# Kernel tuning notes

Measured on AMD Instinct MI355X. Metric: run time of the kernel, lower is better.

## Reference

```python
import jax, jax.numpy as jnp
import numpy as np

N_NODES = 50000
N_EDGES = 1_600_000
F_IN = 128
HID = 64
HEADS = 4
NCLS = 2
NEG_SLOPE = 0.2  # PyG GATConv default


def setup_inputs() -> dict:
    key = jax.random.key(0)
    ks = jax.random.split(key, 12)
    s = 0.1
    return {
        "x": jax.random.normal(ks[0], (N_NODES, F_IN), jnp.float32),
        "edge_index": jax.random.randint(ks[1], (2, N_EDGES), 0, N_NODES, jnp.int32),
        "W1": jax.random.normal(ks[2], (F_IN, HEADS * HID), jnp.float32) * s,
        "att_src1": jax.random.normal(ks[3], (HEADS, HID), jnp.float32) * s,
        "att_dst1": jax.random.normal(ks[4], (HEADS, HID), jnp.float32) * s,
        "b1": jnp.zeros((HEADS * HID,), jnp.float32),
        "W2": jax.random.normal(ks[5], (HEADS * HID, HID), jnp.float32) * s,
        "att_src2": jax.random.normal(ks[6], (1, HID), jnp.float32) * s,
        "att_dst2": jax.random.normal(ks[7], (1, HID), jnp.float32) * s,
        "b2": jnp.zeros((HID,), jnp.float32),
        "Wc": jax.random.normal(ks[8], (HID, NCLS), jnp.float32) * s,
        "bc": jnp.zeros((NCLS,), jnp.float32),
    }


def _gat_layer(x, src, dst, W, a_src, a_dst, bias, heads, out_ch, concat):
    """Faithful PyG GATConv (eval mode): gather, LeakyReLU score, segment softmax by dst, scatter-add."""
    n = x.shape[0]
    h = (x @ W).reshape(n, heads, out_ch)            # [N, H, C]
    alpha_s = (h * a_src).sum(-1)                    # [N, H]
    alpha_d = (h * a_dst).sum(-1)                    # [N, H]
    e = jax.nn.leaky_relu(alpha_s[src] + alpha_d[dst], NEG_SLOPE)  # [E, H]
    e_max = jax.ops.segment_max(e, dst, num_segments=n)
    ex = jnp.exp(e - e_max[dst])
    denom = jax.ops.segment_sum(ex, dst, num_segments=n)
    coef = ex / (denom[dst] + 1e-16)                 # [E, H]
    out = jax.ops.segment_sum(h[src] * coef[:, :, None], dst, num_segments=n)  # [N, H, C]
    out = out.reshape(n, heads * out_ch) if concat else out.mean(axis=1)
    return out + bias


def reference(x, edge_index, W1, att_src1, att_dst1, b1, W2, att_src2, att_dst2, b2, Wc, bc):
    n = x.shape[0]
    loop = jnp.arange(n, dtype=edge_index.dtype)     # GATConv add_self_loops=True
    src = jnp.concatenate([edge_index[0], loop])
    dst = jnp.concatenate([edge_index[1], loop])
    h1 = jax.nn.elu(_gat_layer(x, src, dst, W1, att_src1, att_dst1, b1, HEADS, HID, True))
    # dropout p=0.6 is identity in eval mode
    h2 = jax.nn.elu(_gat_layer(h1, src, dst, W2, att_src2, att_dst2, b2, 1, HID, False))
    pooled = h2.mean(axis=0, keepdims=True)          # batch=None path: [1, HID]
    return pooled @ Wc + bc                          # [1, NCLS]
```

## Files before the change

### kernel.cpp

```cpp
#include <hip/hip_runtime.h>
#include <cstdint>
#include <cstddef>

#define NEG_SLOPE 0.2f
#define F_IN 128
#define C1 256
#define HID 64
#define HEADS 4
#define LOG2E 1.4426950408889634f
#define NBUCK 196
#define BCAP 10240

typedef __attribute__((ext_vector_type(8))) short bf16x8;
typedef __attribute__((ext_vector_type(4))) float f32x4;
typedef __attribute__((ext_vector_type(2))) float f32x2;
typedef unsigned long long ull;

__device__ __forceinline__ float wave_reduce_sum(float v) {
#pragma unroll
  for (int off = 32; off > 0; off >>= 1) v += __shfl_down(v, off);
  return v;
}

__device__ __forceinline__ unsigned short f2bf(float f) {
  union { float f; unsigned int u; } v; v.f = f;
  unsigned int u = v.u;
  unsigned int r = (u + 0x7fffu + ((u >> 16) & 1u)) >> 16;
  return (unsigned short)r;
}

__device__ __forceinline__ unsigned char f2fp8(float f) {
  int p = __builtin_amdgcn_cvt_pk_fp8_f32(f, f, 0, false);
  return (unsigned char)(p & 0xff);
}

__global__ __launch_bounds__(256) void setup_kernel(const float* __restrict__ W1,
                                                    const float* __restrict__ W2,
                                                    unsigned short* __restrict__ W1b,
                                                    unsigned short* __restrict__ W2b,
                                                    int* __restrict__ gcursor,
                                                    float* __restrict__ poolrep) {
  const int TOT = 256 + 4096 + 32768 + 16384;
  for (int idx = threadIdx.x + blockIdx.x * 256; idx < TOT; idx += 256 * gridDim.x) {
    if (idx < 256) {
      gcursor[idx] = 0;
    } else if (idx < 256 + 4096) {
      poolrep[idx - 256] = 0.f;
    } else if (idx < 256 + 4096 + 32768) {
      int o = idx - (256 + 4096);
      int head = o >> 13, ks = (o >> 11) & 3, nt = (o >> 9) & 3;
      int lane = (o >> 3) & 63, j = o & 7;
      int k = ks * 32 + (lane >> 4) * 8 + j;
      int c = head * 64 + nt * 16 + (lane & 15);
      W1b[o] = f2bf(W1[k * 256 + c]);
    } else {
      int o = idx - (256 + 4096 + 32768);
      int ks = o >> 11, nt = (o >> 9) & 3, lane = (o >> 3) & 63, j = o & 7;
      int k = ks * 32 + (lane >> 4) * 8 + j;
      int c = nt * 16 + (lane & 15);
      W2b[o] = f2bf(W2[k * 64 + c]);
    }
  }
}

__global__ __launch_bounds__(256) void gemm1_partition(const float* __restrict__ Af,
                                                       const unsigned short* __restrict__ Wb,
                                                       unsigned char* __restrict__ H8,
                                                       float* __restrict__ as_out,
                                                       float* __restrict__ ad_out,
                                                       const float* __restrict__ att_s,
                                                       const float* __restrict__ att_d,
                                                       int M, int rowblocks,
                                                       const int* __restrict__ esrc,
                                                       const int* __restrict__ edst,
                                                       int* __restrict__ gcursor,
                                                       unsigned* __restrict__ pairs,
                                                       int E, int Etot) {
  __shared__ int hist[256];
  __shared__ int base[256];
  if (blockIdx.x < rowblocks) {
    constexpr int KSTEPS = 4, NH = HEADS, K = 128, N = 256;
    const int lane = threadIdx.x & 63, wid = threadIdx.x >> 6;
    const int rowbase = blockIdx.x * 64 + wid * 16;
    const int g = lane >> 4, li = lane & 15;
    int r_a = rowbase + li;
    if (r_a > M - 1) r_a = M - 1;

    f32x4 acc[NH][4];
#pragma unroll
    for (int h = 0; h < NH; h++)
#pragma unroll
      for (int nt = 0; nt < 4; nt++) {
        acc[h][nt][0] = 0.f; acc[h][nt][1] = 0.f; acc[h][nt][2] = 0.f; acc[h][nt][3] = 0.f;
      }

#pragma unroll
    for (int ks = 0; ks < KSTEPS; ks++) {
      bf16x8 a;
      const float* p = Af + (size_t)r_a * K + ks * 32 + g * 8;
      float4 v0 = *(const float4*)p, v1 = *(const float4*)(p + 4);
      a[0] = (short)f2bf(v0.x); a[1] = (short)f2bf(v0.y);
      a[2] = (short)f2bf(v0.z); a[3] = (short)f2bf(v0.w);
      a[4] = (short)f2bf(v1.x); a[5] = (short)f2bf(v1.y);
      a[6] = (short)f2bf(v1.z); a[7] = (short)f2bf(v1.w);
#pragma unroll
      for (int h = 0; h < NH; h++)
#pragma unroll
        for (int nt = 0; nt < 4; nt++) {
          bf16x8 b = *(const bf16x8*)(Wb + ((size_t)((h * KSTEPS + ks) * 4 + nt) * 64 + lane) * 8);
          acc[h][nt] = __builtin_amdgcn_mfma_f32_16x16x32_bf16(a, b, acc[h][nt], 0, 0, 0);
        }
    }

#pragma unroll
    for (int h = 0; h < NH; h++) {
      float asum[4] = {0.f, 0.f, 0.f, 0.f}, dsum[4] = {0.f, 0.f, 0.f, 0.f};
#pragma unroll
      for (int nt = 0; nt < 4; nt++) {
        float ws = att_s[h * 64 + nt * 16 + li];
        float wd = att_d[h * 64 + nt * 16 + li];
#pragma unroll
        for (int r = 0; r < 4; r++) { asum[r] += acc[h][nt][r] * ws; dsum[r] += acc[h][nt][r] * wd; }
      }
#pragma unroll
      for (int r = 0; r < 4; r++) {
#pragma unroll
        for (int m = 1; m < 16; m <<= 1) {
          asum[r] += __shfl_xor(asum[r], m);
          dsum[r] += __shfl_xor(dsum[r], m);
        }
      }
#pragma unroll
      for (int r = 0; r < 4; r++) {
        int gr = rowbase + g * 4 + r;
        if (gr < M) {
#pragma unroll
          for (int nt = 0; nt < 4; nt++)
            H8[(size_t)gr * N + h * 64 + nt * 16 + li] = f2fp8(acc[h][nt][r]);
          if (li == 0) {
            as_out[(size_t)gr * NH + h] = asum[r] * LOG2E;
            ad_out[(size_t)gr * NH + h] = dsum[r] * LOG2E;
          }
        }
      }
    }
  } else {
    const int tid = threadIdx.x;
    const int e0 = (blockIdx.x - rowblocks) * 2048;
    hist[tid] = 0;
    __syncthreads();
    int d8[8], rk8[8], bk8[8];
#pragma unroll
    for (int j = 0; j < 8; j++) {
      int e = e0 + tid * 8 + j;
      d8[j] = -1;
      if (e < Etot) {
        int d = (e < E) ? edst[e] : (e - E);
        d8[j] = d;
        bk8[j] = d >> 8;
        rk8[j] = atomicAdd(&hist[bk8[j]], 1);
      }
    }
    __syncthreads();
    if (hist[tid] > 0) base[tid] = atomicAdd(&gcursor[tid], hist[tid]);
    __syncthreads();
#pragma unroll
    for (int j = 0; j < 8; j++) {
      int e = e0 + tid * 8 + j;
      if (e < Etot) {
        int s = (e < E) ? esrc[e] : (e - E);
        pairs[(size_t)bk8[j] * BCAP + base[bk8[j]] + rk8[j]] =
            (unsigned)s | ((unsigned)(d8[j] & 255) << 16);
      }
    }
  }
}

__global__ __launch_bounds__(512) void bucket_csr(const unsigned* __restrict__ pairs,
                                                  const int* __restrict__ gcursor,
                                                  const float4* __restrict__ as1,
                                                  const float4* __restrict__ ad1,
                                                  unsigned short* __restrict__ src16,
                                                  ull* __restrict__ w4,
                                                  int* __restrict__ row_ptr,
                                                  int N, int Etot) {
  __shared__ int hist[256], offs[256], cnt2[256], gpre[256];
  const int b = blockIdx.x;
  const int tid = threadIdx.x;
  if (tid < 256) {
    hist[tid] = 0; cnt2[tid] = 0;
    gpre[tid] = (tid < NBUCK) ? gcursor[tid] : 0;
  }
  __syncthreads();
  for (int off = 1; off < 256; off <<= 1) {
    int t = 0;
    if (tid < 256 && tid >= off) t = gpre[tid - off];
    __syncthreads();
    if (tid < 256) gpre[tid] += t;
    __syncthreads();
  }
  const int cnt = gcursor[b];
  const int gbase = (b == 0) ? 0 : gpre[b - 1];
  const unsigned* bp = pairs + (size_t)b * BCAP;
  if (b == 0 && tid == 0) row_ptr[N] = Etot;

  for (int i = tid; i < cnt; i += 512) {
    unsigned p = bp[i];
    atomicAdd(&hist[p >> 16], 1);
  }
  __syncthreads();
  if (tid < 256) offs[tid] = hist[tid];
  __syncthreads();
  for (int off = 1; off < 256; off <<= 1) {
    int t = 0;
    if (tid < 256 && tid >= off) t = offs[tid - off];
    __syncthreads();
    if (tid < 256) offs[tid] += t;
    __syncthreads();
  }
  if (tid < 256) {
    int node = b * 256 + tid;
    if (node < N) row_ptr[node] = gbase + offs[tid] - hist[tid];
  }
  __syncthreads();
  for (int i = tid; i < cnt; i += 512) {
    unsigned p = bp[i];
    int lo = (int)(p >> 16);
    int src = (int)(p & 0xffffu);
    int rank = atomicAdd(&cnt2[lo], 1);
    int pos = gbase + offs[lo] - hist[lo] + rank;
    float4 a = as1[src], dd = ad1[b * 256 + lo];
    float s0 = a.x + dd.x, s1 = a.y + dd.y, s2 = a.z + dd.z, s3 = a.w + dd.w;
    float w0 = exp2f(fmaxf(s0, NEG_SLOPE * s0));
    float w1 = exp2f(fmaxf(s1, NEG_SLOPE * s1));
    float w2 = exp2f(fmaxf(s2, NEG_SLOPE * s2));
    float w3 = exp2f(fmaxf(s3, NEG_SLOPE * s3));
    unsigned w01 = (unsigned)f2bf(w0) | ((unsigned)f2bf(w1) << 16);
    unsigned w23 = (unsigned)f2bf(w2) | ((unsigned)f2bf(w3) << 16);
    src16[pos] = (unsigned short)src;
    w4[pos] = (ull)w01 | ((ull)w23 << 32);
  }
}

__global__ __launch_bounds__(256) void agg1_gemm2(const unsigned char* __restrict__ H8,
                                                  const unsigned short* __restrict__ src16,
                                                  const ull* __restrict__ w4,
                                                  const int* __restrict__ row_ptr,
                                                  const float* __restrict__ b1,
                                                  const unsigned short* __restrict__ W2b,
                                                  const float* __restrict__ att_s2,
                                                  const float* __restrict__ att_d2,
                                                  unsigned char* __restrict__ H2,
                                                  float* __restrict__ as2,
                                                  float* __restrict__ ad2, int n) {
  __shared__ unsigned char lds_h[16 * 512];
  __shared__ float pA[4][16], pD[4][16];
  const int tid = threadIdx.x;
  const int l = tid & 63, w = tid >> 6;
  const int dbase = blockIdx.x * 16;
  const int hh = l >> 4;
  const int shamt = (hh & 1) ? 0 : 16;
  const bool lowpair = hh < 2;
  const float4 bb = *(const float4*)(b1 + l * 4);

#define WSEL(wv) __uint_as_float((((lowpair) ? (unsigned)(wv) : (unsigned)((wv) >> 32)) << shamt) & 0xffff0000u)
#define ACCUM(wgt, u8)                                                     \
  {                                                                        \
    f32x2 lo_ = __builtin_amdgcn_cvt_pk_f32_fp8((int)(u8), false);         \
    f32x2 hi_ = __builtin_amdgcn_cvt_pk_f32_fp8((int)(u8), true);          \
    accA += lo_ * (wgt); accB += hi_ * (wgt);                              \
    denom += (wgt);                                                        \
  }
  for (int i = 0; i < 4; i++) {
    int dloc = w * 4 + i;
    int d = dbase + dloc;
    bool active = d < n;
    f32x2 accA = {0.f, 0.f}, accB = {0.f, 0.f};
    float denom = 0.f;
    if (active) {
      int e0 = __builtin_amdgcn_readfirstlane(row_ptr[d]);
      int e1 = __builtin_amdgcn_readfirstlane(row_ptr[d + 1]);
      int e = e0;
      for (; e + 7 < e1; e += 8) {
        unsigned s0 = src16[e],     s1 = src16[e + 1];
        unsigned s2 = src16[e + 2], s3 = src16[e + 3];
        unsigned s4 = src16[e + 4], s5 = src16[e + 5];
        unsigned s6 = src16[e + 6], s7 = src16[e + 7];
        ull wv0 = w4[e],     wv1 = w4[e + 1], wv2 = w4[e + 2], wv3 = w4[e + 3];
        ull wv4 = w4[e + 4], wv5 = w4[e + 5], wv6 = w4[e + 6], wv7 = w4[e + 7];
        unsigned u0 = *(const unsigned*)(H8 + (size_t)s0 * C1 + l * 4);
        unsigned u1 = *(const unsigned*)(H8 + (size_t)s1 * C1 + l * 4);
        unsigned u2 = *(const unsigned*)(H8 + (size_t)s2 * C1 + l * 4);
        unsigned u3 = *(const unsigned*)(H8 + (size_t)s3 * C1 + l * 4);
        unsigned u4 = *(const unsigned*)(H8 + (size_t)s4 * C1 + l * 4);
        unsigned u5 = *(const unsigned*)(H8 + (size_t)s5 * C1 + l * 4);
        unsigned u6 = *(const unsigned*)(H8 + (size_t)s6 * C1 + l * 4);
        unsigned u7 = *(const unsigned*)(H8 + (size_t)s7 * C1 + l * 4);
        float w0 = WSEL(wv0), w1 = WSEL(wv1), w2 = WSEL(wv2), w3 = WSEL(wv3);
        float w4_ = WSEL(wv4), w5 = WSEL(wv5), w6 = WSEL(wv6), w7 = WSEL(wv7);
        ACCUM(w0, u0) ACCUM(w1, u1) ACCUM(w2, u2) ACCUM(w3, u3)
        ACCUM(w4_, u4) ACCUM(w5, u5) ACCUM(w6, u6) ACCUM(w7, u7)
      }
      for (; e < e1; e++) {
        unsigned s0 = src16[e];
        ull wv = w4[e];
        unsigned u = *(const unsigned*)(H8 + (size_t)s0 * C1 + l * 4);
        float wq = WSEL(wv);
        ACCUM(wq, u)
      }
    }
    float inv = 1.f / (denom + 1e-16f);
    float4 o;
    o.x = accA[0] * inv + bb.x; o.y = accA[1] * inv + bb.y;
    o.z = accB[0] * inv + bb.z; o.w = accB[1] * inv + bb.w;
    o.x = o.x > 0.f ? o.x : (__expf(o.x) - 1.f);
    o.y = o.y > 0.f ? o.y : (__expf(o.y) - 1.f);
    o.z = o.z > 0.f ? o.z : (__expf(o.z) - 1.f);
    o.w = o.w > 0.f ? o.w : (__expf(o.w) - 1.f);
    if (!active) { o.x = 0.f; o.y = 0.f; o.z = 0.f; o.w = 0.f; }
    uint2 pk;
    pk.x = (unsigned int)f2bf(o.x) | ((unsigned int)f2bf(o.y) << 16);
    pk.y = (unsigned int)f2bf(o.z) | ((unsigned int)f2bf(o.w) << 16);
    unsigned byte = (unsigned)(l * 8) ^ ((unsigned)(dloc & 7) << 4);
    *(uint2*)(lds_h + dloc * 512 + byte) = pk;
  }
#undef ACCUM
#undef WSEL
  __syncthreads();

  const int li2 = l & 15, g2 = l >> 4;
  f32x4 acc2;
  acc2[0] = 0.f; acc2[1] = 0.f; acc2[2] = 0.f; acc2[3] = 0.f;
#pragma unroll
  for (int ks = 0; ks < 8; ks++) {
    unsigned byte = (unsigned)((ks * 32 + g2 * 8) * 2) ^ ((unsigned)(li2 & 7) << 4);
    bf16x8 a = *(const bf16x8*)(lds_h + li2 * 512 + byte);
    bf16x8 b = *(const bf16x8*)(W2b + ((size_t)(ks * 4 + w) * 64 + l) * 8);
    acc2 = __builtin_amdgcn_mfma_f32_16x16x32_bf16(a, b, acc2, 0, 0, 0);
  }

  float ws = att_s2[w * 16 + li2], wd = att_d2[w * 16 + li2];
  float asum[4], dsum[4];
#pragma unroll
  for (int r = 0; r < 4; r++) { asum[r] = acc2[r] * ws; dsum[r] = acc2[r] * wd; }
#pragma unroll
  for (int r = 0; r < 4; r++) {
#pragma unroll
    for (int m = 1; m < 16; m <<= 1) {
      asum[r] += __shfl_xor(asum[r], m);
      dsum[r] += __shfl_xor(dsum[r], m);
    }
  }
#pragma unroll
  for (int r = 0; r < 4; r++) {
    int row = g2 * 4 + r;
    int d2 = dbase + row;
    if (d2 < n) H2[(size_t)d2 * HID + w * 16 + li2] = f2fp8(acc2[r]);
    if (li2 == 0) { pA[w][row] = asum[r]; pD[w][row] = dsum[r]; }
  }
  __syncthreads();
  if (tid < 16) {
    int d2 = dbase + tid;
    if (d2 < n) as2[d2] = (pA[0][tid] + pA[1][tid] + pA[2][tid] + pA[3][tid]) * LOG2E;
  } else if (tid < 32) {
    int row = tid - 16;
    int d2 = dbase + row;
    if (d2 < n) ad2[d2] = (pD[0][row] + pD[1][row] + pD[2][row] + pD[3][row]) * LOG2E;
  }
}

__global__ __launch_bounds__(256) void agg2_pool(const unsigned char* __restrict__ H2,
                                                 const float* __restrict__ as_,
                                                 const float* __restrict__ ad_,
                                                 const int* __restrict__ row_ptr,
                                                 const unsigned short* __restrict__ src16,
                                                 const float* __restrict__ b2,
                                                 float* __restrict__ poolrep, int n) {
  __shared__ float lds[4][64];
  int wid = threadIdx.x >> 6;
  int d = blockIdx.x * 4 + wid;
  int l = threadIdx.x & 63, q = l >> 4, li = l & 15;
  float ad = ad_[d];
  int e0 = row_ptr[d], e1 = row_ptr[d + 1];
  f32x2 accA = {0.f, 0.f}, accB = {0.f, 0.f};
  float denom = 0.f;
  int e = e0 + q;
  for (; e + 4 < e1; e += 8) {
    int sa = (int)src16[e];
    int sb = (int)src16[e + 4];
    float sca = as_[sa] + ad, scb = as_[sb] + ad;
    float wa = exp2f(fmaxf(sca, NEG_SLOPE * sca));
    float wb = exp2f(fmaxf(scb, NEG_SLOPE * scb));
    unsigned ua = *(const unsigned*)(H2 + (size_t)sa * HID + li * 4);
    unsigned ub = *(const unsigned*)(H2 + (size_t)sb * HID + li * 4);
    f32x2 loa = __builtin_amdgcn_cvt_pk_f32_fp8((int)ua, false);
    f32x2 hia = __builtin_amdgcn_cvt_pk_f32_fp8((int)ua, true);
    f32x2 lob = __builtin_amdgcn_cvt_pk_f32_fp8((int)ub, false);
    f32x2 hib = __builtin_amdgcn_cvt_pk_f32_fp8((int)ub, true);
    accA += loa * wa; accB += hia * wa;
    accA += lob * wb; accB += hib * wb;
    denom += wa + wb;
  }
  for (; e < e1; e += 4) {
    int s = (int)src16[e];
    float sc = as_[s] + ad;
    float w = exp2f(fmaxf(sc, NEG_SLOPE * sc));
    denom += w;
    unsigned u = *(const unsigned*)(H2 + (size_t)s * HID + li * 4);
    f32x2 lo_ = __builtin_amdgcn_cvt_pk_f32_fp8((int)u, false);
    f32x2 hi_ = __builtin_amdgcn_cvt_pk_f32_fp8((int)u, true);
    accA += lo_ * w; accB += hi_ * w;
  }
#pragma unroll
  for (int m = 16; m <= 32; m <<= 1) {
    accA[0] += __shfl_xor(accA[0], m); accA[1] += __shfl_xor(accA[1], m);
    accB[0] += __shfl_xor(accB[0], m); accB[1] += __shfl_xor(accB[1], m);
    denom += __shfl_xor(denom, m);
  }
  if (q == 0) {
    float inv = 1.f / (denom + 1e-16f);
    float o[4] = {accA[0] * inv + b2[li * 4], accA[1] * inv + b2[li * 4 + 1],
                  accB[0] * inv + b2[li * 4 + 2], accB[1] * inv + b2[li * 4 + 3]};
#pragma unroll
    for (int j = 0; j < 4; j++) {
      float v = o[j];
      lds[wid][li * 4 + j] = v > 0.f ? v : (__expf(v) - 1.f);
    }
  }
  __syncthreads();
  if (threadIdx.x < 64) {
    int c = threadIdx.x;
    float v = lds[0][c] + lds[1][c] + lds[2][c] + lds[3][c];
    atomicAdd(&poolrep[(blockIdx.x & 63) * 64 + c], v);
  }
}

__global__ __launch_bounds__(64) void head_kernel(const float* __restrict__ poolrep,
                                                  const float* __restrict__ Wc,
                                                  const float* __restrict__ bc,
                                                  float* __restrict__ out, float inv_n) {
  int l = threadIdx.x;
  float p = 0.f;
  for (int k = 0; k < 64; k++) p += poolrep[k * 64 + l];
  p *= inv_n;
  float o0 = wave_reduce_sum(p * Wc[l * 2 + 0]);
  float o1 = wave_reduce_sum(p * Wc[l * 2 + 1]);
  if (l == 0) { out[0] = o0 + bc[0]; out[1] = o1 + bc[1]; }
}

static inline size_t align256(size_t x) { return (x + 255) & ~(size_t)255; }

extern "C" void kernel_launch(void* const* d_in, const int* in_sizes, int n_in,
                              void* d_out, int out_size, void* d_ws, size_t ws_size,
                              hipStream_t stream) {
  const float* x        = (const float*)d_in[0];
  const int*   ei       = (const int*)d_in[1];
  const float* W1       = (const float*)d_in[2];
  const float* att_src1 = (const float*)d_in[3];
  const float* att_dst1 = (const float*)d_in[4];
  const float* b1       = (const float*)d_in[5];
  const float* W2       = (const float*)d_in[6];
  const float* att_src2 = (const float*)d_in[7];
  const float* att_dst2 = (const float*)d_in[8];
  const float* b2       = (const float*)d_in[9];
  const float* Wc       = (const float*)d_in[10];
  const float* bc       = (const float*)d_in[11];
  float* out = (float*)d_out;

  const int N = in_sizes[0] / F_IN;
  const int E = in_sizes[1] / 2;
  const int Etot = E + N;
  const int* ei_src = ei;
  const int* ei_dst = ei + E;

  char* w = (char*)d_ws;
  size_t off = 0;
  unsigned char* h1b8 = (unsigned char*)(w + off); off += align256((size_t)N * C1);
  unsigned char* h2b8 = (unsigned char*)(w + off); off += align256((size_t)N * HID);
  float* as1   = (float*)(w + off); off += align256((size_t)N * HEADS * 4);
  float* ad1   = (float*)(w + off); off += align256((size_t)N * HEADS * 4);
  float* as2   = (float*)(w + off); off += align256((size_t)N * 4);
  float* ad2   = (float*)(w + off); off += align256((size_t)N * 4);
  int* row_ptr = (int*)(w + off);   off += align256((size_t)(N + 1) * 4);
  int* gcursor = (int*)(w + off);   off += align256(256 * 4);
  float* poolrep = (float*)(w + off); off += align256(64 * 64 * 4);
  unsigned short* W1b = (unsigned short*)(w + off); off += align256(32768 * 2);
  unsigned short* W2b = (unsigned short*)(w + off); off += align256(16384 * 2);
  unsigned* pairs = (unsigned*)(w + off); off += align256((size_t)NBUCK * BCAP * 4);
  unsigned short* src16 = (unsigned short*)(w + off); off += align256((size_t)Etot * 2);
  ull* w4      = (ull*)(w + off);   off += align256((size_t)Etot * 8);

  int nb4 = (N + 3) / 4;
  int rowblocks = (N + 63) / 64;
  int pblocks = (Etot + 2047) / 2048;
  int fblocks = (N + 15) / 16;

  setup_kernel<<<104, 256, 0, stream>>>(W1, W2, W1b, W2b, gcursor, poolrep);
  gemm1_partition<<<rowblocks + pblocks, 256, 0, stream>>>(
      x, W1b, h1b8, as1, ad1, att_src1, att_dst1, N, rowblocks,
      ei_src, ei_dst, gcursor, pairs, E, Etot);
  bucket_csr<<<NBUCK, 512, 0, stream>>>(pairs, gcursor,
                                        (const float4*)as1, (const float4*)ad1,
                                        src16, w4, row_ptr, N, Etot);
  agg1_gemm2<<<fblocks, 256, 0, stream>>>(h1b8, src16, w4, row_ptr, b1, W2b,
                                          att_src2, att_dst2, h2b8, as2, ad2, N);
  agg2_pool<<<nb4, 256, 0, stream>>>(h2b8, as2, ad2, row_ptr, src16, b2, poolrep, N);
  head_kernel<<<1, 64, 0, stream>>>(poolrep, Wc, bc, out, 1.0f / (float)N);
}
```

Before: 185.1 us.

## Sort each CSR row's edges by source quarter for gather locality

```diff
diff --git a/kernel.cpp b/kernel.cpp
--- a/kernel.cpp
+++ b/kernel.cpp
@@ -176,21 +176,20 @@
   }
 }
 
-__global__ __launch_bounds__(512) void bucket_csr(const unsigned* __restrict__ pairs,
-                                                  const int* __restrict__ gcursor,
-                                                  const float4* __restrict__ as1,
-                                                  const float4* __restrict__ ad1,
-                                                  unsigned short* __restrict__ src16,
-                                                  ull* __restrict__ w4,
-                                                  int* __restrict__ row_ptr,
-                                                  int N, int Etot) {
-  __shared__ int hist[256], offs[256], cnt2[256], gpre[256];
+__global__ __launch_bounds__(1024) void bucket_csr(const unsigned* __restrict__ pairs,
+                                                   const int* __restrict__ gcursor,
+                                                   const float4* __restrict__ as1,
+                                                   const float4* __restrict__ ad1,
+                                                   unsigned short* __restrict__ src16,
+                                                   ull* __restrict__ w4,
+                                                   int* __restrict__ qoff,
+                                                   int N, int Etot) {
+  __shared__ int hist[1024], offs[1024], cnt2[1024], gpre[256];
   const int b = blockIdx.x;
   const int tid = threadIdx.x;
-  if (tid < 256) {
-    hist[tid] = 0; cnt2[tid] = 0;
-    gpre[tid] = (tid < NBUCK) ? gcursor[tid] : 0;
-  }
+  hist[tid] = 0;
+  cnt2[tid] = 0;
+  if (tid < 256) gpre[tid] = (tid < NBUCK) ? gcursor[tid] : 0;
   __syncthreads();
   for (int off = 1; off < 256; off <<= 1) {
     int t = 0;
@@ -202,34 +201,42 @@
   const int cnt = gcursor[b];
   const int gbase = (b == 0) ? 0 : gpre[b - 1];
   const unsigned* bp = pairs + (size_t)b * BCAP;
-  if (b == 0 && tid == 0) row_ptr[N] = Etot;
-
-  for (int i = tid; i < cnt; i += 512) {
+  if (b == 0 && tid == 0) qoff[4 * N] = Etot;
+
+  for (int i = tid; i < cnt; i += 1024) {
     unsigned p = bp[i];
-    atomicAdd(&hist[p >> 16], 1);
-  }
-  __syncthreads();
-  if (tid < 256) offs[tid] = hist[tid];
-  __syncthreads();
-  for (int off = 1; off < 256; off <<= 1) {
-    int t = 0;
-    if (tid < 256 && tid >= off) t = offs[tid - off];
-    __syncthreads();
-    if (tid < 256) offs[tid] += t;
+    int bin = (int)((p >> 16) << 2) | (int)((p & 0xffffu) >> 14);
+    atomicAdd(&hist[bin], 1);
+  }
+  __syncthreads();
+  offs[tid] = hist[tid];
+  __syncthreads();
+  for (int off = 1; off < 1024; off <<= 1) {
+    int t = (tid >= off) ? offs[tid - off] : 0;
+    __syncthreads();
+    offs[tid] += t;
     __syncthreads();
   }
   if (tid < 256) {
     int node = b * 256 + tid;
-    if (node < N) row_ptr[node] = gbase + offs[tid] - hist[tid];
-  }
-  __syncthreads();
-  for (int i = tid; i < cnt; i += 512) {
+    if (node < N) {
+      int4 q;
+      q.x = gbase + offs[tid * 4 + 0] - hist[tid * 4 + 0];
+      q.y = gbase + offs[tid * 4 + 1] - hist[tid * 4 + 1];
+      q.z = gbase + offs[tid * 4 + 2] - hist[tid * 4 + 2];
+      q.w = gbase + offs[tid * 4 + 3] - hist[tid * 4 + 3];
+      *(int4*)(qoff + 4 * node) = q;
+    }
+  }
+  __syncthreads();
+  for (int i = tid; i < cnt; i += 1024) {
     unsigned p = bp[i];
-    int lo = (int)(p >> 16);
+    int dlow = (int)(p >> 16);
     int src = (int)(p & 0xffffu);
-    int rank = atomicAdd(&cnt2[lo], 1);
-    int pos = gbase + offs[lo] - hist[lo] + rank;
-    float4 a = as1[src], dd = ad1[b * 256 + lo];
+    int bin = (dlow << 2) | (src >> 14);
+    int rank = atomicAdd(&cnt2[bin], 1);
+    int pos = gbase + offs[bin] - hist[bin] + rank;
+    float4 a = as1[src], dd = ad1[b * 256 + dlow];
     float s0 = a.x + dd.x, s1 = a.y + dd.y, s2 = a.z + dd.z, s3 = a.w + dd.w;
     float w0 = exp2f(fmaxf(s0, NEG_SLOPE * s0));
     float w1 = exp2f(fmaxf(s1, NEG_SLOPE * s1));
@@ -245,7 +252,7 @@
 __global__ __launch_bounds__(256) void agg1_gemm2(const unsigned char* __restrict__ H8,
                                                   const unsigned short* __restrict__ src16,
                                                   const ull* __restrict__ w4,
-                                                  const int* __restrict__ row_ptr,
+                                                  const int* __restrict__ qoff,
                                                   const float* __restrict__ b1,
                                                   const unsigned short* __restrict__ W2b,
                                                   const float* __restrict__ att_s2,
@@ -278,8 +285,9 @@
     f32x2 accA = {0.f, 0.f}, accB = {0.f, 0.f};
     float denom = 0.f;
     if (active) {
-      int e0 = __builtin_amdgcn_readfirstlane(row_ptr[d]);
-      int e1 = __builtin_amdgcn_readfirstlane(row_ptr[d + 1]);
+      const int* qp = qoff + (size_t)d * 4;
+      int e0 = __builtin_amdgcn_readfirstlane(qp[0]);
+      int e1 = __builtin_amdgcn_readfirstlane(qp[4]);
       int e = e0;
       for (; e + 7 < e1; e += 8) {
         unsigned s0 = src16[e],     s1 = src16[e + 1];
@@ -372,7 +380,7 @@
 __global__ __launch_bounds__(256) void agg2_pool(const unsigned char* __restrict__ H2,
                                                  const float* __restrict__ as_,
                                                  const float* __restrict__ ad_,
-                                                 const int* __restrict__ row_ptr,
+                                                 const int* __restrict__ qoff,
                                                  const unsigned short* __restrict__ src16,
                                                  const float* __restrict__ b2,
                                                  float* __restrict__ poolrep, int n) {
@@ -381,7 +389,9 @@
   int d = blockIdx.x * 4 + wid;
   int l = threadIdx.x & 63, q = l >> 4, li = l & 15;
   float ad = ad_[d];
-  int e0 = row_ptr[d], e1 = row_ptr[d + 1];
+  const int* qp = qoff + (size_t)d * 4;
+  int e0 = __builtin_amdgcn_readfirstlane(qp[0]);
+  int e1 = __builtin_amdgcn_readfirstlane(qp[4]);
   f32x2 accA = {0.f, 0.f}, accB = {0.f, 0.f};
   float denom = 0.f;
   int e = e0 + q;
@@ -481,7 +491,7 @@
   float* ad1   = (float*)(w + off); off += align256((size_t)N * HEADS * 4);
   float* as2   = (float*)(w + off); off += align256((size_t)N * 4);
   float* ad2   = (float*)(w + off); off += align256((size_t)N * 4);
-  int* row_ptr = (int*)(w + off);   off += align256((size_t)(N + 1) * 4);
+  int* qoff    = (int*)(w + off);   off += align256((size_t)(N + 1) * 16);
   int* gcursor = (int*)(w + off);   off += align256(256 * 4);
   float* poolrep = (float*)(w + off); off += align256(64 * 64 * 4);
   unsigned short* W1b = (unsigned short*)(w + off); off += align256(32768 * 2);
@@ -499,11 +509,11 @@
   gemm1_partition<<<rowblocks + pblocks, 256, 0, stream>>>(
       x, W1b, h1b8, as1, ad1, att_src1, att_dst1, N, rowblocks,
       ei_src, ei_dst, gcursor, pairs, E, Etot);
-  bucket_csr<<<NBUCK, 512, 0, stream>>>(pairs, gcursor,
-                                        (const float4*)as1, (const float4*)ad1,
-                                        src16, w4, row_ptr, N, Etot);
-  agg1_gemm2<<<fblocks, 256, 0, stream>>>(h1b8, src16, w4, row_ptr, b1, W2b,
+  bucket_csr<<<NBUCK, 1024, 0, stream>>>(pairs, gcursor,
+                                         (const float4*)as1, (const float4*)ad1,
+                                         src16, w4, qoff, N, Etot);
+  agg1_gemm2<<<fblocks, 256, 0, stream>>>(h1b8, src16, w4, qoff, b1, W2b,
                                           att_src2, att_dst2, h2b8, as2, ad2, N);
-  agg2_pool<<<nb4, 256, 0, stream>>>(h2b8, as2, ad2, row_ptr, src16, b2, poolrep, N);
+  agg2_pool<<<nb4, 256, 0, stream>>>(h2b8, as2, ad2, qoff, src16, b2, poolrep, N);
   head_kernel<<<1, 64, 0, stream>>>(poolrep, Wc, bc, out, 1.0f / (float)N);
 }
```

Result: no change. 186.2 us (+0.6%).

## Halve CSR bucket width and software-pipeline edge index loads in layer-1 aggregation

Applied to the files above, without the earlier changes.

```diff
diff --git a/kernel.cpp b/kernel.cpp
--- a/kernel.cpp
+++ b/kernel.cpp
@@ -8,8 +8,8 @@
 #define HID 64
 #define HEADS 4
 #define LOG2E 1.4426950408889634f
-#define NBUCK 196
-#define BCAP 10240
+#define NBUCK 392
+#define BCAP 5120
 
 typedef __attribute__((ext_vector_type(8))) short bf16x8;
 typedef __attribute__((ext_vector_type(4))) float f32x4;
@@ -40,21 +40,21 @@
                                                     unsigned short* __restrict__ W2b,
                                                     int* __restrict__ gcursor,
                                                     float* __restrict__ poolrep) {
-  const int TOT = 256 + 4096 + 32768 + 16384;
+  const int TOT = 512 + 4096 + 32768 + 16384;
   for (int idx = threadIdx.x + blockIdx.x * 256; idx < TOT; idx += 256 * gridDim.x) {
-    if (idx < 256) {
+    if (idx < 512) {
       gcursor[idx] = 0;
-    } else if (idx < 256 + 4096) {
-      poolrep[idx - 256] = 0.f;
-    } else if (idx < 256 + 4096 + 32768) {
-      int o = idx - (256 + 4096);
+    } else if (idx < 512 + 4096) {
+      poolrep[idx - 512] = 0.f;
+    } else if (idx < 512 + 4096 + 32768) {
+      int o = idx - (512 + 4096);
       int head = o >> 13, ks = (o >> 11) & 3, nt = (o >> 9) & 3;
       int lane = (o >> 3) & 63, j = o & 7;
       int k = ks * 32 + (lane >> 4) * 8 + j;
       int c = head * 64 + nt * 16 + (lane & 15);
       W1b[o] = f2bf(W1[k * 256 + c]);
     } else {
-      int o = idx - (256 + 4096 + 32768);
+      int o = idx - (512 + 4096 + 32768);
       int ks = o >> 11, nt = (o >> 9) & 3, lane = (o >> 3) & 63, j = o & 7;
       int k = ks * 32 + (lane >> 4) * 8 + j;
       int c = nt * 16 + (lane & 15);
@@ -76,8 +76,8 @@
                                                        int* __restrict__ gcursor,
                                                        unsigned* __restrict__ pairs,
                                                        int E, int Etot) {
-  __shared__ int hist[256];
-  __shared__ int base[256];
+  __shared__ int hist[512];
+  __shared__ int base[512];
   if (blockIdx.x < rowblocks) {
     constexpr int KSTEPS = 4, NH = HEADS, K = 128, N = 256;
     const int lane = threadIdx.x & 63, wid = threadIdx.x >> 6;
@@ -147,7 +147,7 @@
   } else {
     const int tid = threadIdx.x;
     const int e0 = (blockIdx.x - rowblocks) * 2048;
-    hist[tid] = 0;
+    hist[tid] = 0; hist[tid + 256] = 0;
     __syncthreads();
     int d8[8], rk8[8], bk8[8];
 #pragma unroll
@@ -157,12 +157,13 @@
       if (e < Etot) {
         int d = (e < E) ? edst[e] : (e - E);
         d8[j] = d;
-        bk8[j] = d >> 8;
+        bk8[j] = d >> 7;
         rk8[j] = atomicAdd(&hist[bk8[j]], 1);
       }
     }
     __syncthreads();
     if (hist[tid] > 0) base[tid] = atomicAdd(&gcursor[tid], hist[tid]);
+    if (hist[tid + 256] > 0) base[tid + 256] = atomicAdd(&gcursor[tid + 256], hist[tid + 256]);
     __syncthreads();
 #pragma unroll
     for (int j = 0; j < 8; j++) {
@@ -170,7 +171,7 @@
       if (e < Etot) {
         int s = (e < E) ? esrc[e] : (e - E);
         pairs[(size_t)bk8[j] * BCAP + base[bk8[j]] + rk8[j]] =
-            (unsigned)s | ((unsigned)(d8[j] & 255) << 16);
+            (unsigned)s | ((unsigned)(d8[j] & 127) << 16);
       }
     }
   }
@@ -184,19 +185,16 @@
                                                   ull* __restrict__ w4,
                                                   int* __restrict__ row_ptr,
                                                   int N, int Etot) {
-  __shared__ int hist[256], offs[256], cnt2[256], gpre[256];
+  __shared__ int hist[128], offs[128], cnt2[128], gpre[512];
   const int b = blockIdx.x;
   const int tid = threadIdx.x;
-  if (tid < 256) {
-    hist[tid] = 0; cnt2[tid] = 0;
-    gpre[tid] = (tid < NBUCK) ? gcursor[tid] : 0;
-  }
-  __syncthreads();
-  for (int off = 1; off < 256; off <<= 1) {
-    int t = 0;
-    if (tid < 256 && tid >= off) t = gpre[tid - off];
-    __syncthreads();
-    if (tid < 256) gpre[tid] += t;
+  if (tid < 128) { hist[tid] = 0; cnt2[tid] = 0; }
+  gpre[tid] = (tid < NBUCK) ? gcursor[tid] : 0;
+  __syncthreads();
+  for (int off = 1; off < 512; off <<= 1) {
+    int t = (tid >= off) ? gpre[tid - off] : 0;
+    __syncthreads();
+    gpre[tid] += t;
     __syncthreads();
   }
   const int cnt = gcursor[b];
@@ -209,17 +207,17 @@
     atomicAdd(&hist[p >> 16], 1);
   }
   __syncthreads();
-  if (tid < 256) offs[tid] = hist[tid];
-  __syncthreads();
-  for (int off = 1; off < 256; off <<= 1) {
+  if (tid < 128) offs[tid] = hist[tid];
+  __syncthreads();
+  for (int off = 1; off < 128; off <<= 1) {
     int t = 0;
-    if (tid < 256 && tid >= off) t = offs[tid - off];
-    __syncthreads();
-    if (tid < 256) offs[tid] += t;
-    __syncthreads();
-  }
-  if (tid < 256) {
-    int node = b * 256 + tid;
+    if (tid < 128 && tid >= off) t = offs[tid - off];
+    __syncthreads();
+    if (tid < 128) offs[tid] += t;
+    __syncthreads();
+  }
+  if (tid < 128) {
+    int node = b * 128 + tid;
     if (node < N) row_ptr[node] = gbase + offs[tid] - hist[tid];
   }
   __syncthreads();
@@ -229,7 +227,7 @@
     int src = (int)(p & 0xffffu);
     int rank = atomicAdd(&cnt2[lo], 1);
     int pos = gbase + offs[lo] - hist[lo] + rank;
-    float4 a = as1[src], dd = ad1[b * 256 + lo];
+    float4 a = as1[src], dd = ad1[b * 128 + lo];
     float s0 = a.x + dd.x, s1 = a.y + dd.y, s2 = a.z + dd.z, s3 = a.w + dd.w;
     float w0 = exp2f(fmaxf(s0, NEG_SLOPE * s0));
     float w1 = exp2f(fmaxf(s1, NEG_SLOPE * s1));
@@ -263,6 +261,11 @@
   const bool lowpair = hh < 2;
   const float4 bb = *(const float4*)(b1 + l * 4);
 
+  const int dw = dbase + w * 4;
+  int bnd[5];
+#pragma unroll
+  for (int j = 0; j < 5; j++) bnd[j] = row_ptr[min(dw + j, n)];
+
 #define WSEL(wv) __uint_as_float((((lowpair) ? (unsigned)(wv) : (unsigned)((wv) >> 32)) << shamt) & 0xffff0000u)
 #define ACCUM(wgt, u8)                                                     \
   {                                                                        \
@@ -278,28 +281,35 @@
     f32x2 accA = {0.f, 0.f}, accB = {0.f, 0.f};
     float denom = 0.f;
     if (active) {
-      int e0 = __builtin_amdgcn_readfirstlane(row_ptr[d]);
-      int e1 = __builtin_amdgcn_readfirstlane(row_ptr[d + 1]);
+      int e0 = __builtin_amdgcn_readfirstlane(bnd[i]);
+      int e1 = __builtin_amdgcn_readfirstlane(bnd[i + 1]);
       int e = e0;
-      for (; e + 7 < e1; e += 8) {
-        unsigned s0 = src16[e],     s1 = src16[e + 1];
-        unsigned s2 = src16[e + 2], s3 = src16[e + 3];
-        unsigned s4 = src16[e + 4], s5 = src16[e + 5];
-        unsigned s6 = src16[e + 6], s7 = src16[e + 7];
-        ull wv0 = w4[e],     wv1 = w4[e + 1], wv2 = w4[e + 2], wv3 = w4[e + 3];
-        ull wv4 = w4[e + 4], wv5 = w4[e + 5], wv6 = w4[e + 6], wv7 = w4[e + 7];
-        unsigned u0 = *(const unsigned*)(H8 + (size_t)s0 * C1 + l * 4);
-        unsigned u1 = *(const unsigned*)(H8 + (size_t)s1 * C1 + l * 4);
-        unsigned u2 = *(const unsigned*)(H8 + (size_t)s2 * C1 + l * 4);
-        unsigned u3 = *(const unsigned*)(H8 + (size_t)s3 * C1 + l * 4);
-        unsigned u4 = *(const unsigned*)(H8 + (size_t)s4 * C1 + l * 4);
-        unsigned u5 = *(const unsigned*)(H8 + (size_t)s5 * C1 + l * 4);
-        unsigned u6 = *(const unsigned*)(H8 + (size_t)s6 * C1 + l * 4);
-        unsigned u7 = *(const unsigned*)(H8 + (size_t)s7 * C1 + l * 4);
-        float w0 = WSEL(wv0), w1 = WSEL(wv1), w2 = WSEL(wv2), w3 = WSEL(wv3);
-        float w4_ = WSEL(wv4), w5 = WSEL(wv5), w6 = WSEL(wv6), w7 = WSEL(wv7);
-        ACCUM(w0, u0) ACCUM(w1, u1) ACCUM(w2, u2) ACCUM(w3, u3)
-        ACCUM(w4_, u4) ACCUM(w5, u5) ACCUM(w6, u6) ACCUM(w7, u7)
+      unsigned sc[8]; ull wc[8];
+      if (e + 8 <= e1) {
+#pragma unroll
+        for (int j = 0; j < 8; j++) { sc[j] = src16[e + j]; wc[j] = w4[e + j]; }
+      }
+      for (; e + 16 <= e1; e += 8) {
+        unsigned sn[8]; ull wn[8];
+#pragma unroll
+        for (int j = 0; j < 8; j++) { sn[j] = src16[e + 8 + j]; wn[j] = w4[e + 8 + j]; }
+#pragma unroll
+        for (int j = 0; j < 8; j++) {
+          unsigned u = *(const unsigned*)(H8 + (size_t)sc[j] * C1 + l * 4);
+          float wq = WSEL(wc[j]);
+          ACCUM(wq, u)
+        }
+#pragma unroll
+        for (int j = 0; j < 8; j++) { sc[j] = sn[j]; wc[j] = wn[j]; }
+      }
+      if (e + 8 <= e1) {
+#pragma unroll
+        for (int j = 0; j < 8; j++) {
+          unsigned u = *(const unsigned*)(H8 + (size_t)sc[j] * C1 + l * 4);
+          float wq = WSEL(wc[j]);
+          ACCUM(wq, u)
+        }
+        e += 8;
       }
       for (; e < e1; e++) {
         unsigned s0 = src16[e];
@@ -381,7 +391,8 @@
   int d = blockIdx.x * 4 + wid;
   int l = threadIdx.x & 63, q = l >> 4, li = l & 15;
   float ad = ad_[d];
-  int e0 = row_ptr[d], e1 = row_ptr[d + 1];
+  int e0 = __builtin_amdgcn_readfirstlane(row_ptr[d]);
+  int e1 = __builtin_amdgcn_readfirstlane(row_ptr[d + 1]);
   f32x2 accA = {0.f, 0.f}, accB = {0.f, 0.f};
   float denom = 0.f;
   int e = e0 + q;
@@ -482,7 +493,7 @@
   float* as2   = (float*)(w + off); off += align256((size_t)N * 4);
   float* ad2   = (float*)(w + off); off += align256((size_t)N * 4);
   int* row_ptr = (int*)(w + off);   off += align256((size_t)(N + 1) * 4);
-  int* gcursor = (int*)(w + off);   off += align256(256 * 4);
+  int* gcursor = (int*)(w + off);   off += align256(512 * 4);
   float* poolrep = (float*)(w + off); off += align256(64 * 64 * 4);
   unsigned short* W1b = (unsigned short*)(w + off); off += align256(32768 * 2);
   unsigned short* W2b = (unsigned short*)(w + off); off += align256(16384 * 2);
```

New measurement: 191.7 us. +3.6%, slower.
